# Kernel optimization log

Hardware: AMD Instinct MI355X
Metric: run time of the kernel (lower is better)

Reference implementation:

```python
import jax, jax.numpy as jnp
import numpy as np

DT = 0.03125                                   # ray-march step size
NSTEPS = int(np.ceil(2.0 * np.sqrt(3.0) / DT)) # enough steps to cross the [-1,1]^3 cube diagonal (=111)


def trilinear_sample(vol, pos):
    """vol: [C, D, Hv, Wv]; pos: [H, W, 3] xyz in [-1,1] (grid_sample convention,
    align_corners=True). Returns [C, H, W]."""
    D, Hv, Wv = vol.shape[1], vol.shape[2], vol.shape[3]

    def axis(g, n):
        g = jnp.clip((g + 1.0) * 0.5 * (n - 1), 0.0, n - 1.0)
        i0 = jnp.minimum(jnp.floor(g).astype(jnp.int32), n - 2)
        return i0, i0 + 1, (g - i0)[None]  # frac broadcast over channel dim

    x0, x1, fx = axis(pos[..., 0], Wv)
    y0, y1, fy = axis(pos[..., 1], Hv)
    z0, z1, fz = axis(pos[..., 2], D)

    def g(z, y, x):
        return vol[:, z, y, x]  # [C, H, W]

    c00 = g(z0, y0, x0) * (1 - fx) + g(z0, y0, x1) * fx
    c01 = g(z0, y1, x0) * (1 - fx) + g(z0, y1, x1) * fx
    c10 = g(z1, y0, x0) * (1 - fx) + g(z1, y0, x1) * fx
    c11 = g(z1, y1, x0) * (1 - fx) + g(z1, y1, x1) * fx
    c0 = c00 * (1 - fy) + c01 * fy
    c1 = c10 * (1 - fy) + c11 * fy
    return c0 * (1 - fz) + c1 * fz


def setup_inputs() -> dict:
    key = jax.random.key(0)
    B, H, W, D = 2, 256, 256, 128
    camrot = jnp.tile(jnp.eye(3, dtype=jnp.float32)[None], (B, 1, 1))
    campos = jnp.tile(jnp.array([[0.0, 0.0, -2.5]], dtype=jnp.float32), (B, 1))
    focal = jnp.full((B, 2), 300.0, dtype=jnp.float32)
    princpt = jnp.full((B, 2), 128.0, dtype=jnp.float32)
    ys, xs = jnp.meshgrid(jnp.arange(H, dtype=jnp.float32),
                          jnp.arange(W, dtype=jnp.float32), indexing='ij')
    pixelcoords = jnp.tile(jnp.stack([xs, ys], axis=-1)[None], (B, 1, 1, 1))
    volume = jax.random.uniform(key, (B, 4, D, D, D), dtype=jnp.float32)
    return dict(camrot=camrot, campos=campos, focal=focal, princpt=princpt,
                pixelcoords=pixelcoords, volume=volume)


def reference(camrot, campos, focal, princpt, pixelcoords, volume):
    # camera rays: pixel -> camera -> world (camrot^T applied, as in torch sum over dim=-2)
    raydir = (pixelcoords - princpt[:, None, None, :]) / focal[:, None, None, :]
    raydir = jnp.concatenate([raydir, jnp.ones_like(raydir[..., :1])], axis=-1)
    raydir = jnp.einsum('bij,bhwi->bhwj', camrot, raydir)
    raydir = raydir / jnp.sqrt(jnp.sum(raydir ** 2, axis=-1, keepdims=True))

    # ray-AABB intersection with [-1,1]^3 (no grad, as in torch.no_grad())
    t1 = (-1.0 - campos[:, None, None, :]) / raydir
    t2 = (1.0 - campos[:, None, None, :]) / raydir
    tmin = jnp.maximum(jnp.minimum(t1[..., 0], t2[..., 0]),
                       jnp.maximum(jnp.minimum(t1[..., 1], t2[..., 1]),
                                   jnp.minimum(t1[..., 2], t2[..., 2])))
    tmax = jnp.minimum(jnp.maximum(t1[..., 0], t2[..., 0]),
                       jnp.minimum(jnp.maximum(t1[..., 1], t2[..., 1]),
                                   jnp.maximum(t1[..., 2], t2[..., 2])))
    hit = tmin < tmax
    t0 = jax.lax.stop_gradient(jnp.maximum(jnp.where(hit, tmin, 0.0), 0.0))

    raypos = campos[:, None, None, :] + raydir * t0[..., None]  # [B,H,W,3]
    B, H, W = raypos.shape[:3]
    rayrgb = jnp.zeros((B, 3, H, W), raypos.dtype)
    rayalpha = jnp.zeros((B, 1, H, W), raypos.dtype)

    def step(carry, _):
        raypos, rayrgb, rayalpha = carry
        valid = jnp.all((raypos > -1.0) & (raypos < 1.0), axis=-1).astype(raypos.dtype)
        samp = jax.vmap(trilinear_sample)(volume, raypos)  # [B,4,H,W]
        contrib = (jnp.minimum(rayalpha + samp[:, 3:4] * DT, 1.0) - rayalpha) * valid[:, None]
        rayrgb = rayrgb + samp[:, :3] * contrib
        rayalpha = rayalpha + contrib
        raypos = raypos + raydir * DT
        return (raypos, rayrgb, rayalpha), None

    (_, rayrgb, rayalpha), _ = jax.lax.scan(step, (raypos, rayrgb, rayalpha),
                                            None, length=NSTEPS)
    return jnp.concatenate([rayrgb, rayalpha], axis=1)  # [B,4,H,W]
```

## Files before the change

### kernel.cpp

```cpp
#include <hip/hip_runtime.h>
#include <math.h>

#pragma clang fp contract(off)

#define DT 0.03125f
#define INV_DT 32.0f
#define NSTEPS 111

#if defined(__has_builtin)
#if __has_builtin(__builtin_amdgcn_udot4)
#define HAVE_UDOT4 1
#endif
#endif

__device__ __forceinline__ unsigned udot4(unsigned a, unsigned b) {
#ifdef HAVE_UDOT4
    return __builtin_amdgcn_udot4(a, b, 0u, false);
#else
    return (a & 0xffu) * (b & 0xffu)
         + ((a >> 8) & 0xffu) * ((b >> 8) & 0xffu)
         + ((a >> 16) & 0xffu) * ((b >> 16) & 0xffu)
         + ((a >> 24) & 0xffu) * ((b >> 24) & 0xffu);
#endif
}

typedef unsigned u32x4 __attribute__((ext_vector_type(4)));


__device__ __forceinline__ unsigned q8(float v) {
    return __float2uint_rn(fminf(fmaxf(v, 0.0f), 1.0f) * 255.0f);
}

template <int DD>
__global__ __launch_bounds__(256) void repack_u8x4_rowshare_kernel(
        const float* __restrict__ vol, uint4* __restrict__ out, long spatial) {
    constexpr int D = DD;
    constexpr int TPR = D / 4;
    constexpr int R = 1024 / D;
    constexpr int ZS = D * D;

    int t = threadIdx.x;
    long b = blockIdx.y;
    long s_base = (long)blockIdx.x << 10;
    int z = (int)(s_base / ZS);
    int rem = (int)(s_base - (long)z * ZS);
    int y0 = rem / D;
    int yl = t / TPR;
    int x0 = (t - yl * TPR) * 4;

    const float* base = vol + b * 4 * spatial + (long)z * ZS;

    __shared__ unsigned stage[4][R + 1][TPR];
    #pragma unroll
    for (int ci = 0; ci < 4; ++ci) {
        const float* p = base + (long)ci * spatial + (y0 + yl) * D + x0;
        float4 v = *(const float4*)p;
        stage[ci][yl][x0 >> 2] =
            q8(v.x) | (q8(v.y) << 8) | (q8(v.z) << 16) | (q8(v.w) << 24);
    }
    if (t < TPR) {
        int ye = y0 + R; if (ye > D - 1) ye = D - 1;
        #pragma unroll
        for (int ci = 0; ci < 4; ++ci) {
            const float* p = base + (long)ci * spatial + ye * D + t * 4;
            float4 v = *(const float4*)p;
            stage[ci][R][t] =
                q8(v.x) | (q8(v.y) << 8) | (q8(v.z) << 16) | (q8(v.w) << 24);
        }
    }
    __syncthreads();

    int w = x0 >> 2;
    bool last = (x0 + 4 >= D);
    uint4 e[4];
    #pragma unroll
    for (int ci = 0; ci < 4; ++ci) {
        unsigned wA0 = stage[ci][yl][w];
        unsigned wB0 = stage[ci][yl + 1][w];
        unsigned a4 = last ? (wA0 >> 24) : (stage[ci][yl][w + 1] & 0xffu);
        unsigned b4 = last ? (wB0 >> 24) : (stage[ci][yl + 1][w + 1] & 0xffu);
        unsigned a[5] = {wA0 & 0xffu, (wA0 >> 8) & 0xffu,
                         (wA0 >> 16) & 0xffu, wA0 >> 24, a4};
        unsigned bb[5] = {wB0 & 0xffu, (wB0 >> 8) & 0xffu,
                          (wB0 >> 16) & 0xffu, wB0 >> 24, b4};
        #pragma unroll
        for (int k = 0; k < 4; ++k) {
            ((unsigned*)&e[k])[ci] =
                a[k] | (a[k + 1] << 8) | (bb[k] << 16) | (bb[k + 1] << 24);
        }
    }

    __shared__ uint4 lds[4 * 257];
    #pragma unroll
    for (int j = 0; j < 4; ++j) lds[j * 257 + t] = e[j];
    __syncthreads();
    uint4* o = out + b * spatial + ((long)blockIdx.x << 10);
    #pragma unroll
    for (int k = 0; k < 4; ++k) {
        o[k * 256 + t] = lds[(t & 3) * 257 + k * 64 + (t >> 2)];
    }
}

__global__ __launch_bounds__(256) void repack_u8x4_lds_kernel(
        const float* __restrict__ vol, uint4* __restrict__ out,
        long spatial, int D) {
    long chunk = (long)blockIdx.x * 256 + threadIdx.x;
    long b = blockIdx.y;
    long s = chunk << 2;
    int zs = D * D;
    int z = (int)(s / zs);
    int rem = (int)(s - (long)z * zs);
    int y = rem / D;
    int x0 = rem - y * D;
    int y1 = (y < D - 1) ? y + 1 : y;
    bool last = (x0 + 4 >= D);

    const float* base = vol + b * 4 * spatial;
    uint4 e[4];
    #pragma unroll
    for (int ci = 0; ci < 4; ++ci) {
        const float* pa = base + (long)ci * spatial + (long)z * zs + y * D + x0;
        const float* pb = base + (long)ci * spatial + (long)z * zs + y1 * D + x0;
        float4 va = *(const float4*)pa;
        float4 vb = *(const float4*)pb;
        float na_sh = __shfl_down(va.x, 1, 64);
        float nb_sh = __shfl_down(vb.x, 1, 64);
        float na = last ? va.w : na_sh;
        float nb = last ? vb.w : nb_sh;
        float ra[5] = {va.x, va.y, va.z, va.w, na};
        float rb[5] = {vb.x, vb.y, vb.z, vb.w, nb};
        #pragma unroll
        for (int k = 0; k < 4; ++k) {
            unsigned d = q8(ra[k]) | (q8(ra[k + 1]) << 8) |
                         (q8(rb[k]) << 16) | (q8(rb[k + 1]) << 24);
            ((unsigned*)&e[k])[ci] = d;
        }
    }

    __shared__ uint4 lds[4 * 257];
    int t = threadIdx.x;
    #pragma unroll
    for (int j = 0; j < 4; ++j) lds[j * 257 + t] = e[j];
    __syncthreads();
    uint4* o = out + b * spatial + ((long)blockIdx.x << 10);
    #pragma unroll
    for (int k = 0; k < 4; ++k) {
        o[k * 256 + t] = lds[(t & 3) * 257 + k * 64 + (t >> 2)];
    }
}

__global__ __launch_bounds__(256) void repack_u8x4_kernel(const float* __restrict__ vol,
                                                          uint4* __restrict__ out,
                                                          long spatial, int D) {
    long chunk = (long)blockIdx.x * blockDim.x + threadIdx.x;
    long nchunks = spatial >> 2;
    if (chunk >= nchunks) return;
    long b = blockIdx.y;
    long s = chunk << 2;
    int zs = D * D;
    int z = (int)(s / zs);
    int rem = (int)(s - (long)z * zs);
    int y = rem / D;
    int x0 = rem - y * D;
    int y1 = (y < D - 1) ? y + 1 : y;

    const float* base = vol + b * 4 * spatial;
    uint4 e[4];
    #pragma unroll
    for (int ci = 0; ci < 4; ++ci) {
        const float* pa = base + (long)ci * spatial + (long)z * zs + y * D + x0;
        const float* pb = base + (long)ci * spatial + (long)z * zs + y1 * D + x0;
        float4 va = *(const float4*)pa;
        float4 vb = *(const float4*)pb;
        bool last = (x0 + 4 >= D);
        float na = last ? pa[3] : pa[4];
        float nb = last ? pb[3] : pb[4];
        float ra[5] = {va.x, va.y, va.z, va.w, na};
        float rb[5] = {vb.x, vb.y, vb.z, vb.w, nb};
        #pragma unroll
        for (int k = 0; k < 4; ++k) {
            unsigned d = q8(ra[k]) | (q8(ra[k + 1]) << 8) |
                         (q8(rb[k]) << 16) | (q8(rb[k + 1]) << 24);
            ((unsigned*)&e[k])[ci] = d;
        }
    }
    uint4* o = out + b * spatial + s;
    o[0] = e[0]; o[1] = e[1]; o[2] = e[2]; o[3] = e[3];
}

__global__ __launch_bounds__(256) void repack_u8_kernel(const float* __restrict__ vol,
                                                        uint4* __restrict__ out,
                                                        long total, long spatial, int D) {
    long idx = (long)blockIdx.x * blockDim.x + threadIdx.x;
    if (idx >= total) return;
    long b = idx / spatial;
    long s = idx - b * spatial;
    int zs = D * D;
    int z = (int)(s / zs);
    int rem = (int)(s - (long)z * zs);
    int y = rem / D;
    int x = rem - y * D;
    int x1 = (x < D - 1) ? x + 1 : x;
    int y1 = (y < D - 1) ? y + 1 : y;
    const float* base = vol + b * 4 * spatial;
    uint4 e;
    #pragma unroll
    for (int ci = 0; ci < 4; ++ci) {
        const float* p = base + (long)ci * spatial + (long)z * zs;
        unsigned d = q8(p[y * D + x]) | (q8(p[y * D + x1]) << 8) |
                     (q8(p[y1 * D + x]) << 16) | (q8(p[y1 * D + x1]) << 24);
        ((unsigned*)&e)[ci] = d;
    }
    out[idx] = e;
}


struct Ray {
    float posx, posy, posz;
    float stx, sty, stz;
    int n;
};

__device__ __forceinline__ Ray ray_setup(const float* __restrict__ camrot,
                                         const float* __restrict__ campos,
                                         const float* __restrict__ focal,
                                         const float* __restrict__ princpt,
                                         const float* __restrict__ pixelcoords,
                                         int b, int y, int x, int H, int W) {
#pragma clang fp contract(off)
    long pidx = (((long)b * H + y) * W + x) * 2;
    float px = pixelcoords[pidx];
    float py = pixelcoords[pidx + 1];
    const float* R = camrot + b * 9;
    float cpx = campos[b * 3 + 0], cpy = campos[b * 3 + 1], cpz = campos[b * 3 + 2];
    float flx = focal[b * 2 + 0], fly = focal[b * 2 + 1];
    float prx = princpt[b * 2 + 0], pry = princpt[b * 2 + 1];

    float rx = (px - prx) / flx;
    float ry = (py - pry) / fly;
    float rz = 1.0f;
    float dx = R[0] * rx + R[3] * ry + R[6] * rz;
    float dy = R[1] * rx + R[4] * ry + R[7] * rz;
    float dz = R[2] * rx + R[5] * ry + R[8] * rz;
    float ss = dx * dx;
    ss = ss + dy * dy;
    ss = ss + dz * dz;
    float nrm = sqrtf(ss);
    dx = dx / nrm; dy = dy / nrm; dz = dz / nrm;

    float t1x = (-1.0f - cpx) / dx, t2x = (1.0f - cpx) / dx;
    float t1y = (-1.0f - cpy) / dy, t2y = (1.0f - cpy) / dy;
    float t1z = (-1.0f - cpz) / dz, t2z = (1.0f - cpz) / dz;
    float tmin = fmaxf(fminf(t1x, t2x), fmaxf(fminf(t1y, t2y), fminf(t1z, t2z)));
    float tmax = fminf(fmaxf(t1x, t2x), fminf(fmaxf(t1y, t2y), fmaxf(t1z, t2z)));
    bool hit = tmin < tmax;
    float t0 = fmaxf(hit ? tmin : 0.0f, 0.0f);

    Ray r;
    r.posx = cpx + dx * t0;
    r.posy = cpy + dy * t0;
    r.posz = cpz + dz * t0;
    r.stx = dx * DT; r.sty = dy * DT; r.stz = dz * DT;

    float span = (tmax - t0) * INV_DT + 4.0f;
    span = fminf(span, (float)NSTEPS);
    r.n = (hit && span > 0.0f) ? (int)span : 0;
    return r;
}


#define ISTEP(C, u)                                                            \
    {                                                                          \
        bool inside = (ipx > -1.0f) && (ipx < 1.0f) && (ipy > -1.0f) &&        \
                      (ipy < 1.0f) && (ipz > -1.0f) && (ipz < 1.0f);           \
        C.m##u = inside ? 1.0f : 0.0f;                                         \
        float gx, gy, gz;                                                      \
        {                                                                      \
            _Pragma("clang fp contract(fast)")                                 \
            gx = ipx * gsc + gsc;                                              \
            gy = ipy * gsc + gsc;                                              \
            gz = ipz * gsc + gsc;                                              \
        }                                                                      \
        int ix = (int)gx; ix = min(max(ix, 0), D - 2);                         \
        int iy = (int)gy; iy = min(max(iy, 0), D - 2);                         \
        int iz = (int)gz; iz = min(max(iz, 0), D - 2);                         \
        float fx = gx - (float)ix;                                             \
        float fy = gy - (float)iy;                                             \
        C.fz##u = gz - (float)iz;                                              \
        unsigned wx1 = (unsigned)(int)(fx * 255.0f + 0.5f);                    \
        unsigned wy1 = (unsigned)(int)(fy * 255.0f + 0.5f);                    \
        unsigned wx0 = 255u - wx1, wy0 = 255u - wy1;                           \
        unsigned p00 = ((wx0 * wy0 + 128u) >> 8) & 0xffu;                      \
        unsigned p10 = ((wx1 * wy0 + 128u) >> 8) & 0xffu;                      \
        unsigned p01 = ((wx0 * wy1 + 128u) >> 8) & 0xffu;                      \
        unsigned p11 = ((wx1 * wy1 + 128u) >> 8) & 0xffu;                      \
        C.wp##u = p00 | (p10 << 8) | (p01 << 16) | (p11 << 24);                \
        unsigned voff = (unsigned)((iz * zs + iy * D + ix) << 4);              \
        asm volatile("global_load_dwordx4 %0, %2, %3\n\t"                      \
                     "global_load_dwordx4 %1, %2, %4"                          \
                     : "=&v"(C.A##u), "=&v"(C.B##u)                            \
                     : "v"(voff), "s"(vp), "s"(vpb)                            \
                     : "memory");                                              \
        ipx = ipx + stx; ipy = ipy + sty; ipz = ipz + stz;                     \
    }

#define CSTEP(C, u)                                                            \
    {                                                                          \
        unsigned wp = C.wp##u;                                                 \
        float rA = (float)udot4(C.A##u[0], wp), rB = (float)udot4(C.B##u[0], wp); \
        float gA = (float)udot4(C.A##u[1], wp), gB = (float)udot4(C.B##u[1], wp); \
        float bA = (float)udot4(C.A##u[2], wp), bB = (float)udot4(C.B##u[2], wp); \
        float sA = (float)udot4(C.A##u[3], wp), sB = (float)udot4(C.B##u[3], wp); \
        float fz = C.fz##u;                                                    \
        float rS, gS, bS, sw;                                                  \
        {                                                                      \
            _Pragma("clang fp contract(fast)")                                 \
            rS = rA + fz * (rB - rA);                                          \
            gS = gA + fz * (gB - gA);                                          \
            bS = bA + fz * (bB - bA);                                          \
            sw = (sA + fz * (sB - sA)) * inv;                                  \
        }                                                                      \
        float contrib = (fminf(alpha + sw * DT, 1.0f) - alpha) * C.m##u;       \
        {                                                                      \
            _Pragma("clang fp contract(fast)")                                 \
            accr = accr + rS * contrib;                                        \
            accg = accg + gS * contrib;                                        \
            accb = accb + bS * contrib;                                        \
        }                                                                      \
        alpha = alpha + contrib;                                               \
        pxx = pxx + stx; pyy = pyy + sty; pzz = pzz + stz;                     \
    }

#define ISSUE_CHUNK(C)   { ISTEP(C, 0) ISTEP(C, 1) ISTEP(C, 2) ISTEP(C, 3) }
#define CONSUME_CHUNK(C) { CSTEP(C, 0) CSTEP(C, 1) CSTEP(C, 2) CSTEP(C, 3) }

#define WAIT_VM8                                                               \
    asm volatile("s_waitcnt vmcnt(8)" ::: "memory");                           \
    __builtin_amdgcn_sched_barrier(0);
#define WAIT_VM0                                                               \
    asm volatile("s_waitcnt vmcnt(0)" ::: "memory");                           \
    __builtin_amdgcn_sched_barrier(0);

#define MARCH_TAIL_STEP                                                        \
    {                                                                          \
        bool inside = (pxx > -1.0f) && (pxx < 1.0f) && (pyy > -1.0f) &&        \
                      (pyy < 1.0f) && (pzz > -1.0f) && (pzz < 1.0f);           \
        float m = inside ? 1.0f : 0.0f;                                        \
        float gx, gy, gz;                                                      \
        {                                                                      \
            _Pragma("clang fp contract(fast)")                                 \
            gx = pxx * gsc + gsc;                                              \
            gy = pyy * gsc + gsc;                                              \
            gz = pzz * gsc + gsc;                                              \
        }                                                                      \
        int ix = (int)gx; ix = min(max(ix, 0), D - 2);                         \
        int iy = (int)gy; iy = min(max(iy, 0), D - 2);                         \
        int iz = (int)gz; iz = min(max(iz, 0), D - 2);                         \
        float fx = gx - (float)ix;                                             \
        float fy = gy - (float)iy;                                             \
        float fz = gz - (float)iz;                                             \
        unsigned wx1 = (unsigned)(int)(fx * 255.0f + 0.5f);                    \
        unsigned wy1 = (unsigned)(int)(fy * 255.0f + 0.5f);                    \
        unsigned wx0 = 255u - wx1, wy0 = 255u - wy1;                           \
        unsigned p00 = ((wx0 * wy0 + 128u) >> 8) & 0xffu;                      \
        unsigned p10 = ((wx1 * wy0 + 128u) >> 8) & 0xffu;                      \
        unsigned p01 = ((wx0 * wy1 + 128u) >> 8) & 0xffu;                      \
        unsigned p11 = ((wx1 * wy1 + 128u) >> 8) & 0xffu;                      \
        unsigned wp = p00 | (p10 << 8) | (p01 << 16) | (p11 << 24);            \
        const u32x4* p_ = vp + (iz * zs + iy * D + ix);                        \
        u32x4 A = p_[0];                                                       \
        u32x4 Bv = p_[zs];                                                     \
        float rA = (float)udot4(A[0], wp), rB = (float)udot4(Bv[0], wp);       \
        float gA = (float)udot4(A[1], wp), gB = (float)udot4(Bv[1], wp);       \
        float bA = (float)udot4(A[2], wp), bB = (float)udot4(Bv[2], wp);       \
        float sA = (float)udot4(A[3], wp), sB = (float)udot4(Bv[3], wp);       \
        float rS, gS, bS, sw;                                                  \
        {                                                                      \
            _Pragma("clang fp contract(fast)")                                 \
            rS = rA + fz * (rB - rA);                                          \
            gS = gA + fz * (gB - gA);                                          \
            bS = bA + fz * (bB - bA);                                          \
            sw = (sA + fz * (sB - sA)) * inv;                                  \
        }                                                                      \
        float contrib = (fminf(alpha + sw * DT, 1.0f) - alpha) * m;            \
        {                                                                      \
            _Pragma("clang fp contract(fast)")                                 \
            accr = accr + rS * contrib;                                        \
            accg = accg + gS * contrib;                                        \
            accb = accb + bS * contrib;                                        \
        }                                                                      \
        alpha = alpha + contrib;                                               \
        pxx = pxx + stx; pyy = pyy + sty; pzz = pzz + stz;                     \
    }

struct Chunk {
    u32x4 A0, A1, A2, A3, B0, B1, B2, B3;
    unsigned wp0, wp1, wp2, wp3;
    float fz0, fz1, fz2, fz3;
    float m0, m1, m2, m3;
};

template <int DD>
__global__ __launch_bounds__(256, 2) void raymarch_dot_kernel(
        const float* __restrict__ camrot, const float* __restrict__ campos,
        const float* __restrict__ focal, const float* __restrict__ princpt,
        const float* __restrict__ pixelcoords, const uint4* __restrict__ vol,
        float* __restrict__ out, int B, int H, int W, int Drt) {
#pragma clang fp contract(off)
    const int D = (DD > 0) ? DD : Drt;
    int x = blockIdx.x * 16 + threadIdx.x;
    int y = blockIdx.y * 16 + threadIdx.y;
    int b = blockIdx.z;
    if (x >= W || y >= H) return;

    Ray r = ray_setup(camrot, campos, focal, princpt, pixelcoords, b, y, x, H, W);

    float accr = 0.0f, accg = 0.0f, accb = 0.0f, alpha = 0.0f;
    const float gsc = 0.5f * (float)(D - 1);
    const float inv = 1.0f / (255.0f * 255.0f);
    const int zs = D * D;
    const u32x4* vp = (const u32x4*)vol + (long)b * ((long)zs * D);
    const u32x4* vpb = vp + zs;
    float pxx = r.posx, pyy = r.posy, pzz = r.posz;
    float ipx = r.posx, ipy = r.posy, ipz = r.posz;
    float stx = r.stx, sty = r.sty, stz = r.stz;

    int nb = r.n & ~3;
    int chunks = nb >> 2;

    WAIT_VM0;

    Chunk c0, c1;
    ISSUE_CHUNK(c0);
    ISSUE_CHUNK(c1);

    int k = 0;
    if (chunks > 0) {
        for (;;) {
            WAIT_VM8;
            CONSUME_CHUNK(c0);
            ++k;
            if (alpha == 1.0f || k >= chunks) break;
            ISSUE_CHUNK(c0);
            WAIT_VM8;
            CONSUME_CHUNK(c1);
            ++k;
            if (alpha == 1.0f || k >= chunks) break;
            ISSUE_CHUNK(c1);
        }
    }
    WAIT_VM0;

    if (alpha != 1.0f) {
        for (int s = k << 2; s < r.n; ++s) { MARCH_TAIL_STEP; }
    }

    long hw = (long)H * W;
    long o = (long)b * 4 * hw + (long)y * W + x;
    out[o] = accr * inv;
    out[o + hw] = accg * inv;
    out[o + 2 * hw] = accb * inv;
    out[o + 3 * hw] = alpha;
}


__global__ __launch_bounds__(256) void raymarch_simple_kernel(
        const float* __restrict__ camrot, const float* __restrict__ campos,
        const float* __restrict__ focal, const float* __restrict__ princpt,
        const float* __restrict__ pixelcoords, const float* __restrict__ vol,
        float* __restrict__ out, int B, int H, int W, int D) {
#pragma clang fp contract(off)
    int x = blockIdx.x * blockDim.x + threadIdx.x;
    int y = blockIdx.y * blockDim.y + threadIdx.y;
    int b = blockIdx.z;
    if (x >= W || y >= H) return;

    Ray r = ray_setup(camrot, campos, focal, princpt, pixelcoords, b, y, x, H, W);

    float accr = 0.0f, accg = 0.0f, accb = 0.0f, alpha = 0.0f;
    float gmax = (float)(D - 1);
    long spatial = (long)D * D * D;
    long zstride = (long)D * D;
    const float* vb = vol + (long)b * 4 * spatial;
    float pxx = r.posx, pyy = r.posy, pzz = r.posz;

    for (int s = 0; s < r.n; ++s) {
        bool inside = (pxx > -1.0f) && (pxx < 1.0f) && (pyy > -1.0f) &&
                      (pyy < 1.0f) && (pzz > -1.0f) && (pzz < 1.0f);
        float m = inside ? 1.0f : 0.0f;
        float gx = fminf(fmaxf((pxx + 1.0f) * 0.5f * gmax, 0.0f), gmax);
        float gy = fminf(fmaxf((pyy + 1.0f) * 0.5f * gmax, 0.0f), gmax);
        float gz = fminf(fmaxf((pzz + 1.0f) * 0.5f * gmax, 0.0f), gmax);
        int ix0 = (int)floorf(gx); if (ix0 > D - 2) ix0 = D - 2;
        int iy0 = (int)floorf(gy); if (iy0 > D - 2) iy0 = D - 2;
        int iz0 = (int)floorf(gz); if (iz0 > D - 2) iz0 = D - 2;
        float fx = gx - (float)ix0;
        float fy = gy - (float)iy0;
        float fz = gz - (float)iz0;

        long s000 = (long)iz0 * zstride + (long)iy0 * D + ix0;
        float c[8][4];
        const long offs[8] = {s000, s000 + 1, s000 + D, s000 + D + 1,
                              s000 + zstride, s000 + zstride + 1,
                              s000 + zstride + D, s000 + zstride + D + 1};
        #pragma unroll
        for (int k = 0; k < 8; ++k) {
            c[k][0] = vb[offs[k]];
            c[k][1] = vb[offs[k] + spatial];
            c[k][2] = vb[offs[k] + 2 * spatial];
            c[k][3] = vb[offs[k] + 3 * spatial];
        }
        float wa = 1.0f - fx, wb = 1.0f - fy, wc = 1.0f - fz;
        float samp[4];
        #pragma unroll
        for (int ci = 0; ci < 4; ++ci) {
            float c00 = c[0][ci] * wa + c[1][ci] * fx;
            float c01 = c[2][ci] * wa + c[3][ci] * fx;
            float c10 = c[4][ci] * wa + c[5][ci] * fx;
            float c11 = c[6][ci] * wa + c[7][ci] * fx;
            float c0 = c00 * wb + c01 * fy;
            float c1 = c10 * wb + c11 * fy;
            samp[ci] = c0 * wc + c1 * fz;
        }
        float contrib = (fminf(alpha + samp[3] * DT, 1.0f) - alpha) * m;
        accr = accr + samp[0] * contrib;
        accg = accg + samp[1] * contrib;
        accb = accb + samp[2] * contrib;
        alpha = alpha + contrib;
        pxx = pxx + r.stx; pyy = pyy + r.sty; pzz = pzz + r.stz;
    }

    long hw = (long)H * W;
    long o = (long)b * 4 * hw + (long)y * W + x;
    out[o] = accr;
    out[o + hw] = accg;
    out[o + 2 * hw] = accb;
    out[o + 3 * hw] = alpha;
}

extern "C" void kernel_launch(void* const* d_in, const int* in_sizes, int n_in,
                              void* d_out, int out_size, void* d_ws, size_t ws_size,
                              hipStream_t stream) {
    const float* camrot = (const float*)d_in[0];
    const float* campos = (const float*)d_in[1];
    const float* focal = (const float*)d_in[2];
    const float* princpt = (const float*)d_in[3];
    const float* pixelcoords = (const float*)d_in[4];
    const float* volume = (const float*)d_in[5];
    float* out = (float*)d_out;

    int B = in_sizes[0] / 9;
    long spatial = (long)in_sizes[5] / (B * 4);
    int D = (int)lround(cbrt((double)spatial));
    while ((long)D * D * D > spatial) D--;
    while ((long)(D + 1) * (D + 1) * (D + 1) <= spatial) D++;
    long hw = (long)in_sizes[4] / (B * 2);
    int H = (int)lround(sqrt((double)hw));
    int W = H;

    size_t vol_bytes = (size_t)B * spatial * sizeof(uint4);

    if (ws_size >= vol_bytes && D >= 2) {
        uint4* vol8 = (uint4*)d_ws;
        long nchunks = spatial >> 2;
        bool rowshare_ok = (D == 128) && ((nchunks % 256) == 0);
        bool lds_ok = ((D & 3) == 0) && ((64 % (D / 4)) == 0) &&
                      ((nchunks % 256) == 0);
        if (rowshare_ok) {
            dim3 rgrd((unsigned)(nchunks / 256), B, 1);
            repack_u8x4_rowshare_kernel<128><<<rgrd, dim3(256), 0, stream>>>(
                volume, vol8, spatial);
        } else if (lds_ok) {
            dim3 rgrd((unsigned)(nchunks / 256), B, 1);
            repack_u8x4_lds_kernel<<<rgrd, dim3(256), 0, stream>>>(volume, vol8,
                                                                   spatial, D);
        } else if ((D & 3) == 0) {
            dim3 rgrd((unsigned)((nchunks + 255) / 256), B, 1);
            repack_u8x4_kernel<<<rgrd, dim3(256), 0, stream>>>(volume, vol8, spatial, D);
        } else {
            long total = (long)B * spatial;
            repack_u8_kernel<<<dim3((unsigned)((total + 255) / 256)), dim3(256), 0,
                               stream>>>(volume, vol8, total, spatial, D);
        }
        dim3 blk(16, 16, 1);
        dim3 grd((W + 15) / 16, (H + 15) / 16, B);
        if (D == 128) {
            raymarch_dot_kernel<128><<<grd, blk, 0, stream>>>(
                camrot, campos, focal, princpt, pixelcoords, vol8, out, B, H, W, D);
        } else {
            raymarch_dot_kernel<0><<<grd, blk, 0, stream>>>(
                camrot, campos, focal, princpt, pixelcoords, vol8, out, B, H, W, D);
        }
    } else {
        dim3 blk(16, 16, 1);
        dim3 grd((W + 15) / 16, (H + 15) / 16, B);
        raymarch_simple_kernel<<<grd, blk, 0, stream>>>(camrot, campos, focal, princpt,
                                                        pixelcoords, volume,
                                                        out, B, H, W, D);
    }
}
```

Measured before the change: 136.1 us.

## Shrink packed volume to x-pair u8 layout and assemble corners with byte perms

```diff
diff --git a/kernel.cpp b/kernel.cpp
--- a/kernel.cpp
+++ b/kernel.cpp
@@ -10,6 +10,9 @@
 #if defined(__has_builtin)
 #if __has_builtin(__builtin_amdgcn_udot4)
 #define HAVE_UDOT4 1
+#endif
+#if __has_builtin(__builtin_amdgcn_perm)
+#define HAVE_PERM 1
 #endif
 #endif
 
@@ -24,194 +27,55 @@
 #endif
 }
 
-typedef unsigned u32x4 __attribute__((ext_vector_type(4)));
+__device__ __forceinline__ unsigned chsel(unsigned hi, unsigned lo, unsigned sel) {
+#ifdef HAVE_PERM
+    return __builtin_amdgcn_perm(hi, lo, sel);
+#else
+    unsigned r = 0;
+    #pragma unroll
+    for (int i = 0; i < 4; ++i) {
+        unsigned sb = (sel >> (8 * i)) & 0xffu;
+        unsigned byte = sb < 4u ? (lo >> (8 * sb)) & 0xffu
+                                : (hi >> (8 * (sb - 4u))) & 0xffu;
+        r |= byte << (8 * i);
+    }
+    return r;
+#endif
+}
+
+typedef unsigned u32x2 __attribute__((ext_vector_type(2)));
 
 
 __device__ __forceinline__ unsigned q8(float v) {
     return __float2uint_rn(fminf(fmaxf(v, 0.0f), 1.0f) * 255.0f);
 }
 
-template <int DD>
-__global__ __launch_bounds__(256) void repack_u8x4_rowshare_kernel(
-        const float* __restrict__ vol, uint4* __restrict__ out, long spatial) {
-    constexpr int D = DD;
-    constexpr int TPR = D / 4;
-    constexpr int R = 1024 / D;
-    constexpr int ZS = D * D;
-
-    int t = threadIdx.x;
+__global__ __launch_bounds__(256) void repack_pair_kernel(
+        const float* __restrict__ vol, u32x2* __restrict__ out,
+        long spatial, int D, long npairs) {
+    long pair = (long)blockIdx.x * 256 + threadIdx.x;
+    if (pair >= npairs) return;
     long b = blockIdx.y;
-    long s_base = (long)blockIdx.x << 10;
-    int z = (int)(s_base / ZS);
-    int rem = (int)(s_base - (long)z * ZS);
-    int y0 = rem / D;
-    int yl = t / TPR;
-    int x0 = (t - yl * TPR) * 4;
-
-    const float* base = vol + b * 4 * spatial + (long)z * ZS;
-
-    __shared__ unsigned stage[4][R + 1][TPR];
+    long s = pair << 1;
+    int x = (int)(s % D);
+
+    const float* base = vol + b * 4 * spatial;
+    unsigned q0[4], q1[4], q2[4];
     #pragma unroll
     for (int ci = 0; ci < 4; ++ci) {
-        const float* p = base + (long)ci * spatial + (y0 + yl) * D + x0;
-        float4 v = *(const float4*)p;
-        stage[ci][yl][x0 >> 2] =
-            q8(v.x) | (q8(v.y) << 8) | (q8(v.z) << 16) | (q8(v.w) << 24);
-    }
-    if (t < TPR) {
-        int ye = y0 + R; if (ye > D - 1) ye = D - 1;
-        #pragma unroll
-        for (int ci = 0; ci < 4; ++ci) {
-            const float* p = base + (long)ci * spatial + ye * D + t * 4;
-            float4 v = *(const float4*)p;
-            stage[ci][R][t] =
-                q8(v.x) | (q8(v.y) << 8) | (q8(v.z) << 16) | (q8(v.w) << 24);
-        }
-    }
-    __syncthreads();
-
-    int w = x0 >> 2;
-    bool last = (x0 + 4 >= D);
-    uint4 e[4];
-    #pragma unroll
-    for (int ci = 0; ci < 4; ++ci) {
-        unsigned wA0 = stage[ci][yl][w];
-        unsigned wB0 = stage[ci][yl + 1][w];
-        unsigned a4 = last ? (wA0 >> 24) : (stage[ci][yl][w + 1] & 0xffu);
-        unsigned b4 = last ? (wB0 >> 24) : (stage[ci][yl + 1][w + 1] & 0xffu);
-        unsigned a[5] = {wA0 & 0xffu, (wA0 >> 8) & 0xffu,
-                         (wA0 >> 16) & 0xffu, wA0 >> 24, a4};
-        unsigned bb[5] = {wB0 & 0xffu, (wB0 >> 8) & 0xffu,
-                          (wB0 >> 16) & 0xffu, wB0 >> 24, b4};
-        #pragma unroll
-        for (int k = 0; k < 4; ++k) {
-            ((unsigned*)&e[k])[ci] =
-                a[k] | (a[k + 1] << 8) | (bb[k] << 16) | (bb[k + 1] << 24);
-        }
-    }
-
-    __shared__ uint4 lds[4 * 257];
-    #pragma unroll
-    for (int j = 0; j < 4; ++j) lds[j * 257 + t] = e[j];
-    __syncthreads();
-    uint4* o = out + b * spatial + ((long)blockIdx.x << 10);
-    #pragma unroll
-    for (int k = 0; k < 4; ++k) {
-        o[k * 256 + t] = lds[(t & 3) * 257 + k * 64 + (t >> 2)];
-    }
-}
-
-__global__ __launch_bounds__(256) void repack_u8x4_lds_kernel(
-        const float* __restrict__ vol, uint4* __restrict__ out,
-        long spatial, int D) {
-    long chunk = (long)blockIdx.x * 256 + threadIdx.x;
-    long b = blockIdx.y;
-    long s = chunk << 2;
-    int zs = D * D;
-    int z = (int)(s / zs);
-    int rem = (int)(s - (long)z * zs);
-    int y = rem / D;
-    int x0 = rem - y * D;
-    int y1 = (y < D - 1) ? y + 1 : y;
-    bool last = (x0 + 4 >= D);
-
-    const float* base = vol + b * 4 * spatial;
-    uint4 e[4];
-    #pragma unroll
-    for (int ci = 0; ci < 4; ++ci) {
-        const float* pa = base + (long)ci * spatial + (long)z * zs + y * D + x0;
-        const float* pb = base + (long)ci * spatial + (long)z * zs + y1 * D + x0;
-        float4 va = *(const float4*)pa;
-        float4 vb = *(const float4*)pb;
-        float na_sh = __shfl_down(va.x, 1, 64);
-        float nb_sh = __shfl_down(vb.x, 1, 64);
-        float na = last ? va.w : na_sh;
-        float nb = last ? vb.w : nb_sh;
-        float ra[5] = {va.x, va.y, va.z, va.w, na};
-        float rb[5] = {vb.x, vb.y, vb.z, vb.w, nb};
-        #pragma unroll
-        for (int k = 0; k < 4; ++k) {
-            unsigned d = q8(ra[k]) | (q8(ra[k + 1]) << 8) |
-                         (q8(rb[k]) << 16) | (q8(rb[k + 1]) << 24);
-            ((unsigned*)&e[k])[ci] = d;
-        }
-    }
-
-    __shared__ uint4 lds[4 * 257];
-    int t = threadIdx.x;
-    #pragma unroll
-    for (int j = 0; j < 4; ++j) lds[j * 257 + t] = e[j];
-    __syncthreads();
-    uint4* o = out + b * spatial + ((long)blockIdx.x << 10);
-    #pragma unroll
-    for (int k = 0; k < 4; ++k) {
-        o[k * 256 + t] = lds[(t & 3) * 257 + k * 64 + (t >> 2)];
-    }
-}
-
-__global__ __launch_bounds__(256) void repack_u8x4_kernel(const float* __restrict__ vol,
-                                                          uint4* __restrict__ out,
-                                                          long spatial, int D) {
-    long chunk = (long)blockIdx.x * blockDim.x + threadIdx.x;
-    long nchunks = spatial >> 2;
-    if (chunk >= nchunks) return;
-    long b = blockIdx.y;
-    long s = chunk << 2;
-    int zs = D * D;
-    int z = (int)(s / zs);
-    int rem = (int)(s - (long)z * zs);
-    int y = rem / D;
-    int x0 = rem - y * D;
-    int y1 = (y < D - 1) ? y + 1 : y;
-
-    const float* base = vol + b * 4 * spatial;
-    uint4 e[4];
-    #pragma unroll
-    for (int ci = 0; ci < 4; ++ci) {
-        const float* pa = base + (long)ci * spatial + (long)z * zs + y * D + x0;
-        const float* pb = base + (long)ci * spatial + (long)z * zs + y1 * D + x0;
-        float4 va = *(const float4*)pa;
-        float4 vb = *(const float4*)pb;
-        bool last = (x0 + 4 >= D);
-        float na = last ? pa[3] : pa[4];
-        float nb = last ? pb[3] : pb[4];
-        float ra[5] = {va.x, va.y, va.z, va.w, na};
-        float rb[5] = {vb.x, vb.y, vb.z, vb.w, nb};
-        #pragma unroll
-        for (int k = 0; k < 4; ++k) {
-            unsigned d = q8(ra[k]) | (q8(ra[k + 1]) << 8) |
-                         (q8(rb[k]) << 16) | (q8(rb[k + 1]) << 24);
-            ((unsigned*)&e[k])[ci] = d;
-        }
-    }
-    uint4* o = out + b * spatial + s;
-    o[0] = e[0]; o[1] = e[1]; o[2] = e[2]; o[3] = e[3];
-}
-
-__global__ __launch_bounds__(256) void repack_u8_kernel(const float* __restrict__ vol,
-                                                        uint4* __restrict__ out,
-                                                        long total, long spatial, int D) {
-    long idx = (long)blockIdx.x * blockDim.x + threadIdx.x;
-    if (idx >= total) return;
-    long b = idx / spatial;
-    long s = idx - b * spatial;
-    int zs = D * D;
-    int z = (int)(s / zs);
-    int rem = (int)(s - (long)z * zs);
-    int y = rem / D;
-    int x = rem - y * D;
-    int x1 = (x < D - 1) ? x + 1 : x;
-    int y1 = (y < D - 1) ? y + 1 : y;
-    const float* base = vol + b * 4 * spatial;
+        const float* p = base + (long)ci * spatial + s;
+        float2 v = *(const float2*)p;
+        float f2 = (x + 2 < D) ? p[2] : p[1];
+        q0[ci] = q8(v.x);
+        q1[ci] = q8(v.y);
+        q2[ci] = q8(f2);
+    }
     uint4 e;
-    #pragma unroll
-    for (int ci = 0; ci < 4; ++ci) {
-        const float* p = base + (long)ci * spatial + (long)z * zs;
-        unsigned d = q8(p[y * D + x]) | (q8(p[y * D + x1]) << 8) |
-                     (q8(p[y1 * D + x]) << 16) | (q8(p[y1 * D + x1]) << 24);
-        ((unsigned*)&e)[ci] = d;
-    }
-    out[idx] = e;
+    e.x = q0[0] | (q1[0] << 8) | (q0[1] << 16) | (q1[1] << 24);
+    e.y = q0[2] | (q1[2] << 8) | (q0[3] << 16) | (q1[3] << 24);
+    e.z = q1[0] | (q2[0] << 8) | (q1[1] << 16) | (q2[1] << 24);
+    e.w = q1[2] | (q2[2] << 8) | (q1[3] << 16) | (q2[3] << 24);
+    *(uint4*)(out + b * spatial + s) = e;
 }
 
 
@@ -295,11 +159,15 @@
         unsigned p01 = ((wx0 * wy1 + 128u) >> 8) & 0xffu;                      \
         unsigned p11 = ((wx1 * wy1 + 128u) >> 8) & 0xffu;                      \
         C.wp##u = p00 | (p10 << 8) | (p01 << 16) | (p11 << 24);                \
-        unsigned voff = (unsigned)((iz * zs + iy * D + ix) << 4);              \
-        asm volatile("global_load_dwordx4 %0, %2, %3\n\t"                      \
-                     "global_load_dwordx4 %1, %2, %4"                          \
-                     : "=&v"(C.A##u), "=&v"(C.B##u)                            \
-                     : "v"(voff), "s"(vp), "s"(vpb)                            \
+        unsigned voffA = (unsigned)((iz * zs + iy * D + ix) << 3);             \
+        unsigned voffB = voffA + (unsigned)(D << 3);                           \
+        asm volatile("global_load_dwordx2 %0, %4, %6\n\t"                      \
+                     "global_load_dwordx2 %1, %5, %6\n\t"                      \
+                     "global_load_dwordx2 %2, %4, %7\n\t"                      \
+                     "global_load_dwordx2 %3, %5, %7"                          \
+                     : "=&v"(C.R0##u), "=&v"(C.R1##u),                         \
+                       "=&v"(C.S0##u), "=&v"(C.S1##u)                          \
+                     : "v"(voffA), "v"(voffB), "s"(vp), "s"(vpb)               \
                      : "memory");                                              \
         ipx = ipx + stx; ipy = ipy + sty; ipz = ipz + stz;                     \
     }
@@ -307,10 +175,15 @@
 #define CSTEP(C, u)                                                            \
     {                                                                          \
         unsigned wp = C.wp##u;                                                 \
-        float rA = (float)udot4(C.A##u[0], wp), rB = (float)udot4(C.B##u[0], wp); \
-        float gA = (float)udot4(C.A##u[1], wp), gB = (float)udot4(C.B##u[1], wp); \
-        float bA = (float)udot4(C.A##u[2], wp), bB = (float)udot4(C.B##u[2], wp); \
-        float sA = (float)udot4(C.A##u[3], wp), sB = (float)udot4(C.B##u[3], wp); \
+        u32x2 r0 = C.R0##u, r1 = C.R1##u, s0 = C.S0##u, s1 = C.S1##u;          \
+        float rA = (float)udot4(chsel(r1[0], r0[0], 0x05040100u), wp);         \
+        float gA = (float)udot4(chsel(r1[0], r0[0], 0x07060302u), wp);         \
+        float bA = (float)udot4(chsel(r1[1], r0[1], 0x05040100u), wp);         \
+        float sA = (float)udot4(chsel(r1[1], r0[1], 0x07060302u), wp);         \
+        float rB = (float)udot4(chsel(s1[0], s0[0], 0x05040100u), wp);         \
+        float gB = (float)udot4(chsel(s1[0], s0[0], 0x07060302u), wp);         \
+        float bB = (float)udot4(chsel(s1[1], s0[1], 0x05040100u), wp);         \
+        float sB = (float)udot4(chsel(s1[1], s0[1], 0x07060302u), wp);         \
         float fz = C.fz##u;                                                    \
         float rS, gS, bS, sw;                                                  \
         {                                                                      \
@@ -334,8 +207,8 @@
 #define ISSUE_CHUNK(C)   { ISTEP(C, 0) ISTEP(C, 1) ISTEP(C, 2) ISTEP(C, 3) }
 #define CONSUME_CHUNK(C) { CSTEP(C, 0) CSTEP(C, 1) CSTEP(C, 2) CSTEP(C, 3) }
 
-#define WAIT_VM8                                                               \
-    asm volatile("s_waitcnt vmcnt(8)" ::: "memory");                           \
+#define WAIT_VM16                                                              \
+    asm volatile("s_waitcnt vmcnt(16)" ::: "memory");                          \
     __builtin_amdgcn_sched_barrier(0);
 #define WAIT_VM0                                                               \
     asm volatile("s_waitcnt vmcnt(0)" ::: "memory");                           \
@@ -367,13 +240,19 @@
         unsigned p01 = ((wx0 * wy1 + 128u) >> 8) & 0xffu;                      \
         unsigned p11 = ((wx1 * wy1 + 128u) >> 8) & 0xffu;                      \
         unsigned wp = p00 | (p10 << 8) | (p01 << 16) | (p11 << 24);            \
-        const u32x4* p_ = vp + (iz * zs + iy * D + ix);                        \
-        u32x4 A = p_[0];                                                       \
-        u32x4 Bv = p_[zs];                                                     \
-        float rA = (float)udot4(A[0], wp), rB = (float)udot4(Bv[0], wp);       \
-        float gA = (float)udot4(A[1], wp), gB = (float)udot4(Bv[1], wp);       \
-        float bA = (float)udot4(A[2], wp), bB = (float)udot4(Bv[2], wp);       \
-        float sA = (float)udot4(A[3], wp), sB = (float)udot4(Bv[3], wp);       \
+        const u32x2* e_ = vp + (iz * zs + iy * D + ix);                        \
+        u32x2 r0 = e_[0];                                                      \
+        u32x2 r1 = e_[D];                                                      \
+        u32x2 s0 = e_[zs];                                                     \
+        u32x2 s1 = e_[zs + D];                                                 \
+        float rA = (float)udot4(chsel(r1[0], r0[0], 0x05040100u), wp);         \
+        float gA = (float)udot4(chsel(r1[0], r0[0], 0x07060302u), wp);         \
+        float bA = (float)udot4(chsel(r1[1], r0[1], 0x05040100u), wp);         \
+        float sA = (float)udot4(chsel(r1[1], r0[1], 0x07060302u), wp);         \
+        float rB = (float)udot4(chsel(s1[0], s0[0], 0x05040100u), wp);         \
+        float gB = (float)udot4(chsel(s1[0], s0[0], 0x07060302u), wp);         \
+        float bB = (float)udot4(chsel(s1[1], s0[1], 0x05040100u), wp);         \
+        float sB = (float)udot4(chsel(s1[1], s0[1], 0x07060302u), wp);         \
         float rS, gS, bS, sw;                                                  \
         {                                                                      \
             _Pragma("clang fp contract(fast)")                                 \
@@ -394,7 +273,10 @@
     }
 
 struct Chunk {
-    u32x4 A0, A1, A2, A3, B0, B1, B2, B3;
+    u32x2 R00, R01, R02, R03;
+    u32x2 R10, R11, R12, R13;
+    u32x2 S00, S01, S02, S03;
+    u32x2 S10, S11, S12, S13;
     unsigned wp0, wp1, wp2, wp3;
     float fz0, fz1, fz2, fz3;
     float m0, m1, m2, m3;
@@ -404,7 +286,7 @@
 __global__ __launch_bounds__(256, 2) void raymarch_dot_kernel(
         const float* __restrict__ camrot, const float* __restrict__ campos,
         const float* __restrict__ focal, const float* __restrict__ princpt,
-        const float* __restrict__ pixelcoords, const uint4* __restrict__ vol,
+        const float* __restrict__ pixelcoords, const u32x2* __restrict__ vol,
         float* __restrict__ out, int B, int H, int W, int Drt) {
 #pragma clang fp contract(off)
     const int D = (DD > 0) ? DD : Drt;
@@ -419,8 +301,8 @@
     const float gsc = 0.5f * (float)(D - 1);
     const float inv = 1.0f / (255.0f * 255.0f);
     const int zs = D * D;
-    const u32x4* vp = (const u32x4*)vol + (long)b * ((long)zs * D);
-    const u32x4* vpb = vp + zs;
+    const u32x2* vp = vol + (long)b * ((long)zs * D);
+    const u32x2* vpb = vp + zs;
     float pxx = r.posx, pyy = r.posy, pzz = r.posz;
     float ipx = r.posx, ipy = r.posy, ipz = r.posz;
     float stx = r.stx, sty = r.sty, stz = r.stz;
@@ -437,12 +319,12 @@
     int k = 0;
     if (chunks > 0) {
         for (;;) {
-            WAIT_VM8;
+            WAIT_VM16;
             CONSUME_CHUNK(c0);
             ++k;
             if (alpha == 1.0f || k >= chunks) break;
             ISSUE_CHUNK(c0);
-            WAIT_VM8;
+            WAIT_VM16;
             CONSUME_CHUNK(c1);
             ++k;
             if (alpha == 1.0f || k >= chunks) break;
@@ -558,30 +440,14 @@
     int H = (int)lround(sqrt((double)hw));
     int W = H;
 
-    size_t vol_bytes = (size_t)B * spatial * sizeof(uint4);
-
-    if (ws_size >= vol_bytes && D >= 2) {
-        uint4* vol8 = (uint4*)d_ws;
-        long nchunks = spatial >> 2;
-        bool rowshare_ok = (D == 128) && ((nchunks % 256) == 0);
-        bool lds_ok = ((D & 3) == 0) && ((64 % (D / 4)) == 0) &&
-                      ((nchunks % 256) == 0);
-        if (rowshare_ok) {
-            dim3 rgrd((unsigned)(nchunks / 256), B, 1);
-            repack_u8x4_rowshare_kernel<128><<<rgrd, dim3(256), 0, stream>>>(
-                volume, vol8, spatial);
-        } else if (lds_ok) {
-            dim3 rgrd((unsigned)(nchunks / 256), B, 1);
-            repack_u8x4_lds_kernel<<<rgrd, dim3(256), 0, stream>>>(volume, vol8,
-                                                                   spatial, D);
-        } else if ((D & 3) == 0) {
-            dim3 rgrd((unsigned)((nchunks + 255) / 256), B, 1);
-            repack_u8x4_kernel<<<rgrd, dim3(256), 0, stream>>>(volume, vol8, spatial, D);
-        } else {
-            long total = (long)B * spatial;
-            repack_u8_kernel<<<dim3((unsigned)((total + 255) / 256)), dim3(256), 0,
-                               stream>>>(volume, vol8, total, spatial, D);
-        }
+    size_t vol_bytes = (size_t)B * spatial * sizeof(u32x2);
+
+    if (ws_size >= vol_bytes && D >= 2 && (D & 1) == 0) {
+        u32x2* vol8 = (u32x2*)d_ws;
+        long npairs = spatial >> 1;
+        dim3 rgrd((unsigned)((npairs + 255) / 256), B, 1);
+        repack_pair_kernel<<<rgrd, dim3(256), 0, stream>>>(volume, vol8,
+                                                           spatial, D, npairs);
         dim3 blk(16, 16, 1);
         dim3 grd((W + 15) / 16, (H + 15) / 16, B);
         if (D == 128) {
```

After: 138.0 us. About the same (+1.4%).
